# Kernel tuning notes

Hardware: AMD Instinct MI355X
Metric: run time of the kernel (lower is better)

Reference implementation:

```python
import jax, jax.numpy as jnp
from jax import lax
import numpy as np

H = 64          # featureDim (conv channels)
BN_EPS = 1e-5
COS_EPS = 1e-8


def _conv_block(x, w, b, g, beta):
    # Conv(k3, valid) + BatchNorm(batch stats, training mode) + ReLU + MaxPool2
    y = lax.conv_general_dilated(x, w, (1, 1), 'VALID',
                                 dimension_numbers=('NCHW', 'OIHW', 'NCHW'))
    y = y + b[None, :, None, None]
    mu = jnp.mean(y, axis=(0, 2, 3), keepdims=True)
    var = jnp.var(y, axis=(0, 2, 3), keepdims=True)
    y = (y - mu) * lax.rsqrt(var + BN_EPS) * g[None, :, None, None] + beta[None, :, None, None]
    y = jax.nn.relu(y)
    return lax.reduce_window(y, -jnp.inf, lax.max, (1, 1, 2, 2), (1, 1, 2, 2), 'VALID')


def _lstm_dir(xs, Wi, Wh, bi, bh, h, c):
    # one direction of nn.LSTM, batch size 1 (state vectors of shape [H])
    def step(carry, x):
        h, c = carry
        gates = x @ Wi.T + h @ Wh.T + bi + bh          # [4H], pytorch gate order i,f,g,o
        i_, f_, g_, o_ = jnp.split(gates, 4)
        c = jax.nn.sigmoid(f_) * c + jax.nn.sigmoid(i_) * jnp.tanh(g_)
        h = jax.nn.sigmoid(o_) * jnp.tanh(c)
        return (h, c), h
    _, hs = lax.scan(step, (h, c), xs)
    return hs  # [N, H]


def setup_inputs() -> dict:
    key = jax.random.key(0)
    ks = jax.random.split(key, 32)
    N, T, WAY = 1024, 1024, 20
    d = {}
    d['trainIm'] = jax.random.normal(ks[0], (N, 1, 28, 28), jnp.float32)
    d['trainLabel'] = jax.random.uniform(ks[1], (N, WAY), dtype=jnp.float32)
    d['testIm'] = jax.random.normal(ks[2], (T, 1, 28, 28), jnp.float32)
    d['testLabel'] = jax.random.uniform(ks[3], (T, WAY), dtype=jnp.float32)
    # featureNet params
    d['c1w'] = jax.random.normal(ks[4], (H, 1, 3, 3), jnp.float32) * 0.3
    d['c1b'] = jax.random.normal(ks[5], (H,), jnp.float32) * 0.05
    d['bn1g'] = jnp.ones((H,), jnp.float32)
    d['bn1b'] = jnp.zeros((H,), jnp.float32)
    d['c2w'] = jax.random.normal(ks[6], (H, H, 3, 3), jnp.float32) * 0.05
    d['c2b'] = jax.random.normal(ks[7], (H,), jnp.float32) * 0.05
    d['bn2g'] = jnp.ones((H,), jnp.float32)
    d['bn2b'] = jnp.zeros((H,), jnp.float32)
    d['c3w'] = jax.random.normal(ks[8], (H, H, 3, 3), jnp.float32) * 0.05
    d['c3b'] = jax.random.normal(ks[9], (H,), jnp.float32) * 0.05
    d['bn3g'] = jnp.ones((H,), jnp.float32)
    d['bn3b'] = jnp.zeros((H,), jnp.float32)
    # bidirectional nn.LSTM(H, H) params
    d['wi_f'] = jax.random.normal(ks[10], (4 * H, H), jnp.float32) * 0.1
    d['wh_f'] = jax.random.normal(ks[11], (4 * H, H), jnp.float32) * 0.1
    d['bi_f'] = jax.random.normal(ks[12], (4 * H,), jnp.float32) * 0.05
    d['bh_f'] = jax.random.normal(ks[13], (4 * H,), jnp.float32) * 0.05
    d['wi_b'] = jax.random.normal(ks[14], (4 * H, H), jnp.float32) * 0.1
    d['wh_b'] = jax.random.normal(ks[15], (4 * H, H), jnp.float32) * 0.1
    d['bi_b'] = jax.random.normal(ks[16], (4 * H,), jnp.float32) * 0.05
    d['bh_b'] = jax.random.normal(ks[17], (4 * H,), jnp.float32) * 0.05
    d['h0'] = jax.random.normal(ks[18], (2, 1, H), jnp.float32)
    d['c0'] = jax.random.normal(ks[19], (2, 1, H), jnp.float32)
    # AttenLSTMCell params + attLSTM initial state
    d['att_wih'] = jax.random.normal(ks[20], (H, 4 * H), jnp.float32) * 0.1
    d['att_whh'] = jax.random.normal(ks[21], (2 * H, 4 * H), jnp.float32) * 0.1
    d['att_b'] = jnp.zeros((4 * H,), jnp.float32)
    d['att_h0'] = jax.random.normal(ks[22], (1, H), jnp.float32)
    d['att_c0'] = jax.random.normal(ks[23], (1, H), jnp.float32)
    d['att_r0'] = jax.random.normal(ks[24], (1, H), jnp.float32)
    return d


def reference(trainIm, trainLabel, testIm, testLabel,
              c1w, c1b, bn1g, bn1b, c2w, c2b, bn2g, bn2b, c3w, c3b, bn3g, bn3b,
              wi_f, wh_f, bi_f, bh_f, wi_b, wh_b, bi_b, bh_b, h0, c0,
              att_wih, att_whh, att_b, att_h0, att_c0, att_r0):
    def feat(x):
        y = _conv_block(x, c1w, c1b, bn1g, bn1b)
        y = _conv_block(y, c2w, c2b, bn2g, bn2b)
        y = _conv_block(y, c3w, c3b, bn3g, bn3b)   # [B, 64, 1, 1]
        return y.reshape(-1, H)                    # [B, 64]

    ftr = feat(trainIm)   # [N, 64]
    fte = feat(testIm)    # [T, 64]

    # getCondEmbed_G: BiLSTM; cond[i] = fw[i] + bw_out[N-1-i] + x[i] == fw[i] + bw_raw[i] + x[i]
    hf = _lstm_dir(ftr, wi_f, wh_f, bi_f, bh_f, h0[0, 0], c0[0, 0])
    hb_raw = _lstm_dir(ftr[::-1], wi_b, wh_b, bi_b, bh_b, h0[1, 0], c0[1, 0])
    cond_train = hf + hb_raw + ftr                 # [N, 64]

    # getCondEmbed_F: sequential attLSTM over test samples (state persists across samples)
    def att_step(carry, x):
        h, c, r = carry                            # each [64]
        hcat = jnp.concatenate([h, r])             # [128]
        gates = hcat @ att_whh + x @ att_wih + att_b   # [256], cell gate order f,i,o,g
        f_, i_, o_, g_ = jnp.split(gates, 4)
        c = jax.nn.sigmoid(f_) * c + jax.nn.sigmoid(i_) * jnp.tanh(g_)
        h = jax.nn.sigmoid(o_) * jnp.tanh(c) + x   # residual add of testF
        att = jax.nn.softmax(cond_train @ h)       # [N] attention over support set
        r = att @ cond_train                       # [64] read vector
        return (h, c, r), h

    _, cond_test = lax.scan(att_step, (att_h0[0], att_c0[0], att_r0[0]), fte)  # [T, 64]

    # getLabel: cosine-similarity softmax attention over support labels
    num = cond_test @ cond_train.T                                       # [T, N]
    den = jnp.linalg.norm(cond_test, axis=1)[:, None] * jnp.linalg.norm(cond_train, axis=1)[None, :]
    sim = num / jnp.maximum(den, COS_EPS)
    att = jax.nn.softmax(sim, axis=1)
    return att @ trainLabel                                              # [T, way]
```

## Files before the change

### kernel.cpp

```cpp
#include <hip/hip_runtime.h>
#include <stdint.h>

__device__ __forceinline__ float bf2f(uint16_t v){ return __uint_as_float(((uint32_t)v) << 16); }
__device__ __forceinline__ uint16_t f2bf(float x){
  uint32_t u = __float_as_uint(x);
  return (uint16_t)((u + 0x7fffu + ((u >> 16) & 1u)) >> 16);
}
__device__ __forceinline__ float sigf(float x){
  float cx = fminf(fmaxf(x, -88.f), 88.f);
  return 1.f/(1.f + expf(-cx));
}
__device__ __forceinline__ float tanh_s(float x){
  float cx = fminf(fmaxf(x, -44.f), 44.f);
  return tanhf(cx);
}
__device__ __forceinline__ float fast_sig(float x){
  float cx = fminf(fmaxf(x, -60.f), 60.f);
  return 1.f/(1.f + __expf(-cx));
}
__device__ __forceinline__ float fast_tanh(float x){
  float cx = fminf(fmaxf(x, -15.f), 15.f);
  float e = __expf(2.f*cx);
  return (e - 1.f)/(e + 1.f);
}

typedef float v16 __attribute__((ext_vector_type(16)));

__device__ __forceinline__ float dot16(v16 v, const float4* p){
  float4 a = p[0], b = p[1], c = p[2], d = p[3];
  float s0 = v.s0*a.x + v.s1*a.y + v.s2*a.z + v.s3*a.w;
  float s1 = v.s4*b.x + v.s5*b.y + v.s6*b.z + v.s7*b.w;
  float s2 = v.s8*c.x + v.s9*c.y + v.sa*c.z + v.sb*c.w;
  float s3 = v.sc*d.x + v.sd*d.y + v.se*d.z + v.sf*d.w;
  return (s0+s1)+(s2+s3);
}
__device__ __forceinline__ void dot16pair(v16 va, v16 vb, const float4* p,
                                          float& accA, float& accB){
  float4 a = p[0], b = p[1], c = p[2], d = p[3];
  accA += (va.s0*a.x + va.s1*a.y + va.s2*a.z + va.s3*a.w)
        + (va.s4*b.x + va.s5*b.y + va.s6*b.z + va.s7*b.w)
        + (va.s8*c.x + va.s9*c.y + va.sa*c.z + va.sb*c.w)
        + (va.sc*d.x + va.sd*d.y + va.se*d.z + va.sf*d.w);
  accB += (vb.s0*a.x + vb.s1*a.y + vb.s2*a.z + vb.s3*a.w)
        + (vb.s4*b.x + vb.s5*b.y + vb.s6*b.z + vb.s7*b.w)
        + (vb.s8*c.x + vb.s9*c.y + vb.sa*c.z + vb.sb*c.w)
        + (vb.sc*d.x + vb.sd*d.y + vb.se*d.z + vb.sf*d.w);
}

#define LD16S(dst, P) do{ \
  dst.s0=(P)[0];    dst.s1=(P)[256];  dst.s2=(P)[512];  dst.s3=(P)[768];  \
  dst.s4=(P)[1024]; dst.s5=(P)[1280]; dst.s6=(P)[1536]; dst.s7=(P)[1792]; \
  dst.s8=(P)[2048]; dst.s9=(P)[2304]; dst.sa=(P)[2560]; dst.sb=(P)[2816]; \
  dst.sc=(P)[3072]; dst.sd=(P)[3328]; dst.se=(P)[3584]; dst.sf=(P)[3840]; }while(0)
#define LD16SB(dst, P) do{ \
  dst.s0=bf2f((P)[0]);    dst.s1=bf2f((P)[256]);  dst.s2=bf2f((P)[512]);  dst.s3=bf2f((P)[768]);  \
  dst.s4=bf2f((P)[1024]); dst.s5=bf2f((P)[1280]); dst.s6=bf2f((P)[1536]); dst.s7=bf2f((P)[1792]); \
  dst.s8=bf2f((P)[2048]); dst.s9=bf2f((P)[2304]); dst.sa=bf2f((P)[2560]); dst.sb=bf2f((P)[2816]); \
  dst.sc=bf2f((P)[3072]); dst.sd=bf2f((P)[3328]); dst.se=bf2f((P)[3584]); dst.sf=bf2f((P)[3840]); }while(0)
#define LD16CB(dst, P) do{ \
  dst.s0=bf2f((P)[0]);  dst.s1=bf2f((P)[1]);  dst.s2=bf2f((P)[2]);  dst.s3=bf2f((P)[3]);  \
  dst.s4=bf2f((P)[4]);  dst.s5=bf2f((P)[5]);  dst.s6=bf2f((P)[6]);  dst.s7=bf2f((P)[7]);  \
  dst.s8=bf2f((P)[8]);  dst.s9=bf2f((P)[9]);  dst.sa=bf2f((P)[10]); dst.sb=bf2f((P)[11]); \
  dst.sc=bf2f((P)[12]); dst.sd=bf2f((P)[13]); dst.se=bf2f((P)[14]); dst.sf=bf2f((P)[15]); }while(0)

static const size_t OFF_STATS = 0;
static const size_t OFF_FLAG  = 3072;
static const size_t OFF_AB    = 4096;
static const size_t OFF_P2R   = 8192;
static const size_t OFF_Y3    = 13115392;
static const size_t OFF_F     = 17833984;
static const size_t OFF_XI    = 18358272;
static const size_t OFF_XATT  = 20455424;
static const size_t OFF_CA    = 21504000;
static const size_t OFF_CB    = 21766144;
static const size_t OFF_COND  = 22028288;
static const size_t OFF_NC    = 22290432;
static const size_t OFF_CT    = 22294528;

__global__ void k_sniff(const uint32_t* im, float* stats, int* flag){
  int t = threadIdx.x;
  for (int i = t; i < 768; i += 256) stats[i] = 0.f;
  if (t < 64){
    uint32_t w = im[t];
    uint32_t e = (w >> 7) & 0xffu;
    bool sane = (e >= 100u && e <= 140u);
    unsigned long long m = __ballot(sane);
    if (t == 0) flag[0] = (__popcll(m) < 48) ? 1 : 0;
  }
}

__global__ __launch_bounds__(256) void k_conv1_stats(const void* im0, const void* im1,
        const void* w1, const void* b1, float* stats, const int* flag){
  __shared__ float xs[784];
  __shared__ float wl[576];
  __shared__ float bl1[64];
  __shared__ float rs[256], rq[256];
  int img = blockIdx.x;
  bool f32 = flag[0] != 0;
  if (f32){
    const float* im = (img < 1024) ? ((const float*)im0 + img*784) : ((const float*)im1 + (img-1024)*784);
    for (int i = threadIdx.x; i < 784; i += 256) xs[i] = im[i];
    for (int i = threadIdx.x; i < 576; i += 256) wl[i] = ((const float*)w1)[i];
    if (threadIdx.x < 64) bl1[threadIdx.x] = ((const float*)b1)[threadIdx.x];
  } else {
    const uint16_t* im = (img < 1024) ? ((const uint16_t*)im0 + img*784) : ((const uint16_t*)im1 + (img-1024)*784);
    for (int i = threadIdx.x; i < 784; i += 256) xs[i] = bf2f(im[i]);
    for (int i = threadIdx.x; i < 576; i += 256) wl[i] = bf2f(((const uint16_t*)w1)[i]);
    if (threadIdx.x < 64) bl1[threadIdx.x] = bf2f(((const uint16_t*)b1)[threadIdx.x]);
  }
  __syncthreads();
  int c = threadIdx.x & 63, pg = threadIdx.x >> 6;
  float w[9];
  #pragma unroll
  for (int k = 0; k < 9; k++) w[k] = wl[c*9+k];
  float bias = bl1[c];
  float s = 0.f, q = 0.f;
  for (int pos = pg; pos < 676; pos += 4){
    int y = pos/26, x = pos - y*26;
    const float* p = xs + y*28 + x;
    float acc = bias;
    #pragma unroll
    for (int dy = 0; dy < 3; dy++)
      #pragma unroll
      for (int dx = 0; dx < 3; dx++)
        acc += w[dy*3+dx]*p[dy*28+dx];
    s += acc; q += acc*acc;
  }
  rs[threadIdx.x] = s; rq[threadIdx.x] = q;
  __syncthreads();
  if (threadIdx.x < 64){
    float S = rs[c] + rs[c+64] + rs[c+128] + rs[c+192];
    float Q = rq[c] + rq[c+64] + rq[c+128] + rq[c+192];
    int batch = img >> 10;
    atomicAdd(&stats[batch*128 + c*2 + 0], S);
    atomicAdd(&stats[batch*128 + c*2 + 1], Q);
  }
}

__global__ void k_bnfin(const float* stats, float* ab, const void* g, const void* be,
                        int layer, float invc, const int* flag){
  __shared__ float gl[64], bel[64];
  int t = threadIdx.x;
  bool f32 = flag[0] != 0;
  if (t < 64){
    if (f32){ gl[t] = ((const float*)g)[t]; bel[t] = ((const float*)be)[t]; }
    else    { gl[t] = bf2f(((const uint16_t*)g)[t]); bel[t] = bf2f(((const uint16_t*)be)[t]); }
  }
  __syncthreads();
  if (t >= 128) return;
  int batch = t >> 6, c = t & 63;
  float s = stats[layer*256 + batch*128 + c*2];
  float q = stats[layer*256 + batch*128 + c*2 + 1];
  float mu = s*invc;
  float var = fmaxf(q*invc - mu*mu, 0.f);
  float A = gl[c] * rsqrtf(var + 1e-5f);
  float B = bel[c] - mu*A;
  ab[layer*256 + batch*128 + c*2]     = A;
  ab[layer*256 + batch*128 + c*2 + 1] = B;
}

__global__ __launch_bounds__(256) void k_conv2(const void* im0, const void* im1,
        const void* w1, const void* b1, const float* ab,
        const void* w2, const void* c2b, float* p2raw, float* stats, const int* flag){
  __shared__ float img[10816];
  __shared__ float ovl[4608];
  __shared__ float cbias[64];
  int b = blockIdx.x;
  int tid = threadIdx.x;
  bool f32 = flag[0] != 0;
  if (f32){
    const float* im = (b < 1024) ? ((const float*)im0 + b*784) : ((const float*)im1 + (b-1024)*784);
    for (int i = tid; i < 784; i += 256) ovl[i] = im[i];
    for (int i = tid; i < 576; i += 256) ovl[784+i] = ((const float*)w1)[i];
    if (tid < 64){ ovl[1360+tid] = ((const float*)b1)[tid]; cbias[tid] = ((const float*)c2b)[tid]; }
  } else {
    const uint16_t* im = (b < 1024) ? ((const uint16_t*)im0 + b*784) : ((const uint16_t*)im1 + (b-1024)*784);
    for (int i = tid; i < 784; i += 256) ovl[i] = bf2f(im[i]);
    for (int i = tid; i < 576; i += 256) ovl[784+i] = bf2f(((const uint16_t*)w1)[i]);
    if (tid < 64){ ovl[1360+tid] = bf2f(((const uint16_t*)b1)[tid]); cbias[tid] = bf2f(((const uint16_t*)c2b)[tid]); }
  }
  __syncthreads();
  int c = tid & 63, pg = tid >> 6;
  int batch = b >> 10;
  {
    float w[9];
    #pragma unroll
    for (int k = 0; k < 9; k++) w[k] = ovl[784 + c*9 + k];
    float bias = ovl[1360 + c];
    float A = ab[batch*128 + c*2], B = ab[batch*128 + c*2 + 1];
    for (int pp = pg; pp < 169; pp += 4){
      int py = pp/13, px = pp - py*13;
      float m = 0.f;
      #pragma unroll
      for (int q = 0; q < 4; q++){
        int yy = 2*py + (q>>1), xx = 2*px + (q&1);
        const float* p = ovl + yy*28 + xx;
        float acc = bias;
        #pragma unroll
        for (int dy = 0; dy < 3; dy++)
          #pragma unroll
          for (int dx = 0; dx < 3; dx++)
            acc += w[dy*3+dx]*p[dy*28+dx];
        m = fmaxf(m, A*acc + B);
      }
      img[c*169 + pp] = m;
    }
  }
  int lane = tid & 63, wv = tid >> 6;
  int pos0 = lane;
  int pos1 = lane + 64;
  bool v1 = (pos1 < 121);
  int p1c = v1 ? pos1 : pos0;
  int y0 = pos0/11, x0 = pos0 - y0*11;
  int y1 = p1c/11,  x1 = p1c - y1*11;
  float acc0[16], acc1[16];
  #pragma unroll
  for (int cc = 0; cc < 16; cc++){ acc0[cc]=0.f; acc1[cc]=0.f; }
  for (int ch = 0; ch < 8; ch++){
    int ci0 = ch*8;
    __syncthreads();
    if (f32){
      for (int i = tid; i < 4608; i += 256){
        int co = i/72, r = i - co*72;
        ovl[i] = ((const float*)w2)[(co*64 + ci0)*9 + r];
      }
    } else {
      for (int i = tid; i < 4608; i += 256){
        int co = i/72, r = i - co*72;
        ovl[i] = bf2f(((const uint16_t*)w2)[(co*64 + ci0)*9 + r]);
      }
    }
    __syncthreads();
    for (int cil = 0; cil < 8; cil++){
      int ci = ci0 + cil;
      float a[9], bv[9];
      const float* q0 = img + ci*169 + y0*13 + x0;
      const float* q1 = img + ci*169 + y1*13 + x1;
      #pragma unroll
      for (int dy = 0; dy < 3; dy++)
        #pragma unroll
        for (int dx = 0; dx < 3; dx++){
          a[dy*3+dx]  = q0[dy*13+dx];
          bv[dy*3+dx] = q1[dy*13+dx];
        }
      #pragma unroll
      for (int cc = 0; cc < 16; cc++){
        const float* wp = ovl + (wv*16+cc)*72 + cil*9;
        #pragma unroll
        for (int k = 0; k < 9; k++){
          acc0[cc] += wp[k]*a[k];
          acc1[cc] += wp[k]*bv[k];
        }
      }
    }
  }
  __syncthreads();
  float* ybuf = img;
  #pragma unroll
  for (int cc = 0; cc < 16; cc++){
    int co = wv*16 + cc;
    float bs = cbias[co];
    float u0 = acc0[cc] + bs;
    float u1 = acc1[cc] + bs;
    ybuf[co*121 + pos0] = u0;
    if (v1) ybuf[co*121 + pos1] = u1;
    float s = u0 + (v1 ? u1 : 0.f);
    float q = u0*u0 + (v1 ? u1*u1 : 0.f);
    #pragma unroll
    for (int off = 32; off; off >>= 1){
      s += __shfl_down(s, off);
      q += __shfl_down(q, off);
    }
    if (lane == 0){
      atomicAdd(&stats[256 + batch*128 + co*2 + 0], s);
      atomicAdd(&stats[256 + batch*128 + co*2 + 1], q);
    }
  }
  __syncthreads();
  for (int idx = tid; idx < 1600; idx += 256){
    int cc = idx/25, pp = idx - cc*25;
    int py = pp/5, px = pp - py*5;
    const float* s = ybuf + cc*121;
    float m = fmaxf(fmaxf(s[(2*py)*11 + 2*px], s[(2*py)*11 + 2*px + 1]),
                    fmaxf(s[(2*py+1)*11 + 2*px], s[(2*py+1)*11 + 2*px + 1]));
    p2raw[(size_t)b*1600 + idx] = m;
  }
}

__global__ __launch_bounds__(256) void k_conv3(const float* p2raw, const float* ab,
        const void* w3, const void* c3b, float* y3, float* stats, const int* flag){
  __shared__ float pimg[12800];
  __shared__ float wch[2304];
  __shared__ float cb3[64];
  __shared__ float abl[128];
  __shared__ float lstat[128];
  int b = blockIdx.x;
  int tid = threadIdx.x;
  bool f32 = flag[0] != 0;
  int batch = (b*8) >> 10;
  if (tid < 128){ abl[tid] = ab[256 + batch*128 + tid]; lstat[tid] = 0.f; }
  if (f32){ if (tid >= 128 && tid < 192) cb3[tid-128] = ((const float*)c3b)[tid-128]; }
  else    { if (tid >= 128 && tid < 192) cb3[tid-128] = bf2f(((const uint16_t*)c3b)[tid-128]); }
  __syncthreads();
  for (int idx = tid; idx < 12800; idx += 256){
    int rem = idx & 1599;
    int cch = rem / 25;
    pimg[idx] = fmaxf(abl[cch*2]*p2raw[(size_t)b*12800 + idx] + abl[cch*2+1], 0.f);
  }
  int il = tid >> 5, sub = tid & 31;
  float acc[18];
  #pragma unroll
  for (int s = 0; s < 18; s++){
    int o = sub + s*32;
    acc[s] = cb3[o/9];
  }
  for (int ch = 0; ch < 16; ch++){
    int ci0 = ch*4;
    __syncthreads();
    if (f32){
      for (int i = tid; i < 2304; i += 256){
        int co = i/36, r = i - co*36;
        wch[i] = ((const float*)w3)[(co*64 + ci0)*9 + r];
      }
    } else {
      for (int i = tid; i < 2304; i += 256){
        int co = i/36, r = i - co*36;
        wch[i] = bf2f(((const uint16_t*)w3)[(co*64 + ci0)*9 + r]);
      }
    }
    __syncthreads();
    #pragma unroll
    for (int s = 0; s < 18; s++){
      int o = sub + s*32;
      int co = o/9, pos = o - co*9;
      int y = pos/3, x = pos - y*3;
      float a = acc[s];
      #pragma unroll
      for (int cil = 0; cil < 4; cil++){
        const float* p = pimg + il*1600 + (ci0+cil)*25 + y*5 + x;
        const float* w = wch + co*36 + cil*9;
        #pragma unroll
        for (int dy = 0; dy < 3; dy++)
          #pragma unroll
          for (int dx = 0; dx < 3; dx++)
            a += w[dy*3+dx]*p[dy*5+dx];
      }
      acc[s] = a;
    }
  }
  #pragma unroll
  for (int s = 0; s < 18; s++){
    int o = sub + s*32;
    int co = o/9;
    y3[(size_t)(b*8+il)*576 + o] = acc[s];
    atomicAdd(&lstat[co*2 + 0], acc[s]);
    atomicAdd(&lstat[co*2 + 1], acc[s]*acc[s]);
  }
  __syncthreads();
  if (tid < 128)
    atomicAdd(&stats[512 + batch*128 + tid], lstat[tid]);
}

__global__ __launch_bounds__(256) void k_pool3(const float* y3, const float* ab, float* ff){
  int idx = blockIdx.x*256 + threadIdx.x;
  int img = idx >> 6, c = idx & 63;
  int batch = img >> 10;
  float A = ab[512 + batch*128 + c*2], B = ab[512 + batch*128 + c*2 + 1];
  const float* p = y3 + (size_t)img*576 + c*9;
  float m = 0.f;
  m = fmaxf(m, A*p[0]+B);
  m = fmaxf(m, A*p[1]+B);
  m = fmaxf(m, A*p[3]+B);
  m = fmaxf(m, A*p[4]+B);
  ff[idx] = m;
}

__global__ __launch_bounds__(256) void k_xproj(const float* ff,
        const void* wi_f, const void* bi_f, const void* bh_f,
        const void* wi_b, const void* bi_b, const void* bh_b,
        const void* att_wih, const void* att_b,
        float* Xi, float* Xatt, const int* flag){
  int which = blockIdx.x >> 10, t = blockIdx.x & 1023;
  __shared__ float xv[64];
  bool f32 = flag[0] != 0;
  const float* row = (which == 0) ? ff + t*64
                   : (which == 1) ? ff + (1023 - t)*64
                   : ff + (1024 + t)*64;
  if (threadIdx.x < 64) xv[threadIdx.x] = row[threadIdx.x];
  __syncthreads();
  int j = threadIdx.x;
  if (which < 2){
    const void* wi = which ? wi_b : wi_f;
    const void* bi = which ? bi_b : bi_f;
    const void* bh = which ? bh_b : bh_f;
    float acc;
    if (f32){
      acc = ((const float*)bi)[j] + ((const float*)bh)[j];
      const float* wp = (const float*)wi + j*64;
      #pragma unroll 8
      for (int k = 0; k < 64; k++) acc += wp[k]*xv[k];
    } else {
      acc = bf2f(((const uint16_t*)bi)[j]) + bf2f(((const uint16_t*)bh)[j]);
      const uint16_t* wp = (const uint16_t*)wi + j*64;
      #pragma unroll 8
      for (int k = 0; k < 64; k++) acc += bf2f(wp[k])*xv[k];
    }
    Xi[(size_t)which*262144 + t*256 + j] = acc;
  } else {
    float acc;
    if (f32){
      acc = ((const float*)att_b)[j];
      for (int k = 0; k < 64; k++) acc += ((const float*)att_wih)[k*256 + j]*xv[k];
    } else {
      acc = bf2f(((const uint16_t*)att_b)[j]);
      for (int k = 0; k < 64; k++) acc += bf2f(((const uint16_t*)att_wih)[k*256 + j])*xv[k];
    }
    Xatt[t*256 + j] = acc;
  }
}

__global__ __launch_bounds__(256, 1) void k_bilstm(const void* wh_f, const void* wh_b,
        const void* h0, const void* c0, const float* Xi, float* condA, float* condB,
        const int* flag){
  int dir = blockIdx.x;
  int j = threadIdx.x;
  bool f32 = flag[0] != 0;
  v16 wa, wb, wc, wd;
  if (f32){
    const v16* wp = (const v16*)((const float*)(dir ? wh_b : wh_f) + j*64);
    wa = wp[0]; wb = wp[1]; wc = wp[2]; wd = wp[3];
  } else {
    const uint16_t* wp = (const uint16_t*)(dir ? wh_b : wh_f) + j*64;
    LD16CB(wa, wp); LD16CB(wb, wp+16); LD16CB(wc, wp+32); LD16CB(wd, wp+48);
  }
  __shared__ __align__(16) float h[64];
  __shared__ float ga[256];
  float c = 0.f;
  if (j < 64){
    if (f32){ h[j] = ((const float*)h0)[dir*64 + j]; c = ((const float*)c0)[dir*64 + j]; }
    else    { h[j] = bf2f(((const uint16_t*)h0)[dir*64 + j]); c = bf2f(((const uint16_t*)c0)[dir*64 + j]); }
  }
  __syncthreads();
  const float* X = Xi + (size_t)dir*262144;
  float* out = dir ? condB : condA;
  float xcur = X[j];
  for (int t = 0; t < 1024; t++){
    float xnext = (t < 1023) ? X[(t+1)*256 + j] : 0.f;
    const float4* hp = (const float4*)h;
    float g = xcur + dot16(wa, hp) + dot16(wb, hp+4) + dot16(wc, hp+8) + dot16(wd, hp+12);
    ga[j] = (j < 128 || j >= 192) ? fast_sig(g) : fast_tanh(g);
    __syncthreads();
    if (j < 64){
      c = ga[64+j]*c + ga[j]*ga[128+j];
      float hv = ga[192+j]*fast_tanh(c);
      h[j] = hv;
      out[t*64 + j] = hv;
    }
    xcur = xnext;
    __syncthreads();
  }
}

__global__ void k_cond(const float* condA, const float* condB, const float* ff,
                       float* cond, float* ncond){
  int t = blockIdx.x, j = threadIdx.x;
  float v = condA[t*64+j] + condB[t*64+j] + ff[t*64+j];
  cond[t*64+j] = v;
  float s = v*v;
  #pragma unroll
  for (int off = 32; off; off >>= 1) s += __shfl_down(s, off);
  if (j == 0) ncond[t] = sqrtf(s);
}

__device__ __forceinline__ void av_chunk(v16 pv, int ch, int tid,
        float* pbuf, float (*rs2)[544]){
  float* pb = pbuf + tid*17;
  pb[0]=pv.s0;  pb[1]=pv.s1;  pb[2]=pv.s2;  pb[3]=pv.s3;
  pb[4]=pv.s4;  pb[5]=pv.s5;  pb[6]=pv.s6;  pb[7]=pv.s7;
  pb[8]=pv.s8;  pb[9]=pv.s9;  pb[10]=pv.sa; pb[11]=pv.sb;
  pb[12]=pv.sc; pb[13]=pv.sd; pb[14]=pv.se; pb[15]=pv.sf;
  __syncthreads();
  int kk = tid & 15, seg = tid >> 4;
  float a = 0.f;
  #pragma unroll
  for (int q = 0; q < 16; q++)
    a += pbuf[(seg*16+q)*17 + kk];
  rs2[ch][seg*17 + kk] = a;
  __syncthreads();
}

__global__ __launch_bounds__(512, 1) void k_attlstm(
        const float* cond, const float* Xatt, const float* ff,
        const void* whh, const void* ah0, const void* ac0, const void* ar0,
        float* ctest, const int* flag){
  __shared__ __align__(16) float hr[128];
  __shared__ float gpart[512];
  __shared__ float pbuf[512*17];
  __shared__ float rs2[4][544];
  __shared__ float wred[16];
  int tid = threadIdx.x;
  bool f32 = flag[0] != 0;
  int j = tid & 255, half = tid >> 8;
  v16 wka, wkb, wkc, wkd;
  if (f32){
    const float* W = (const float*)whh + (size_t)half*16384 + j;
    LD16S(wka, W); LD16S(wkb, W+4096); LD16S(wkc, W+8192); LD16S(wkd, W+12288);
  } else {
    const uint16_t* W = (const uint16_t*)whh + (size_t)half*16384 + j;
    LD16SB(wka, W); LD16SB(wkb, W+4096); LD16SB(wkc, W+8192); LD16SB(wkd, W+12288);
  }
  const v16* rp0 = (const v16*)(cond + (size_t)tid*64);
  const v16* rp1 = (const v16*)(cond + (size_t)(tid+512)*64);
  v16 r0a = rp0[0], r0b = rp0[1], r0c = rp0[2], r0d = rp0[3];
  v16 r1a = rp1[0], r1b = rp1[1], r1c = rp1[2], r1d = rp1[3];
  float c = 0.f;
  if (f32){
    if (tid < 64){ hr[tid] = ((const float*)ah0)[tid]; c = ((const float*)ac0)[tid]; }
    else if (tid < 128) hr[tid] = ((const float*)ar0)[tid-64];
  } else {
    if (tid < 64){ hr[tid] = bf2f(((const uint16_t*)ah0)[tid]); c = bf2f(((const uint16_t*)ac0)[tid]); }
    else if (tid < 128) hr[tid] = bf2f(((const uint16_t*)ar0)[tid-64]);
  }
  __syncthreads();
  int lane = tid & 63, wv = tid >> 6;
  const float* fte = ff + 65536;
  for (int st = 0; st < 1024; st++){
    {
      const float4* hc = (const float4*)(hr + half*64);
      float g = (half == 0) ? Xatt[st*256 + j] : 0.f;
      g += dot16(wka, hc) + dot16(wkb, hc+4) + dot16(wkc, hc+8) + dot16(wkd, hc+12);
      gpart[tid] = g;
    }
    __syncthreads();
    if (tid < 64){
      float xres = fte[st*64 + tid];
      float gf = gpart[tid]     + gpart[256+tid];
      float gi = gpart[64+tid]  + gpart[320+tid];
      float go = gpart[128+tid] + gpart[384+tid];
      float gg = gpart[192+tid] + gpart[448+tid];
      float f_ = fast_sig(gf), i_ = fast_sig(gi), o_ = fast_sig(go), g_ = fast_tanh(gg);
      c = f_*c + i_*g_;
      float hv = o_*fast_tanh(c) + xres;
      hr[tid] = hv;
      ctest[st*64 + tid] = hv;
    }
    __syncthreads();
    float lg0 = 0.f, lg1 = 0.f;
    {
      const float4* hq = (const float4*)hr;
      dot16pair(r0a, r1a, hq,    lg0, lg1);
      dot16pair(r0b, r1b, hq+4,  lg0, lg1);
      dot16pair(r0c, r1c, hq+8,  lg0, lg1);
      dot16pair(r0d, r1d, hq+12, lg0, lg1);
    }
    float mx = fmaxf(lg0, lg1);
    #pragma unroll
    for (int off = 32; off; off >>= 1) mx = fmaxf(mx, __shfl_xor(mx, off));
    if (lane == 0) wred[wv] = mx;
    __syncthreads();
    float gmax = fmaxf(fmaxf(fmaxf(wred[0],wred[1]),fmaxf(wred[2],wred[3])),
                       fmaxf(fmaxf(wred[4],wred[5]),fmaxf(wred[6],wred[7])));
    float e0 = __expf(lg0 - gmax), e1 = __expf(lg1 - gmax);
    float s = e0 + e1;
    #pragma unroll
    for (int off = 32; off; off >>= 1) s += __shfl_xor(s, off);
    if (lane == 0) wred[8+wv] = s;
    __syncthreads();
    float inv = 1.f/(((wred[8]+wred[9])+(wred[10]+wred[11]))
                   + ((wred[12]+wred[13])+(wred[14]+wred[15])));
    av_chunk(e0*r0a + e1*r1a, 0, tid, pbuf, rs2);
    av_chunk(e0*r0b + e1*r1b, 1, tid, pbuf, rs2);
    av_chunk(e0*r0c + e1*r1c, 2, tid, pbuf, rs2);
    av_chunk(e0*r0d + e1*r1d, 3, tid, pbuf, rs2);
    if (tid < 64){
      int kk = lane & 15, chq = lane >> 4;
      float a = 0.f;
      #pragma unroll
      for (int sgm = 0; sgm < 32; sgm++) a += rs2[chq][sgm*17 + kk];
      hr[64 + lane] = a * inv;
    }
    __syncthreads();
  }
}

__global__ __launch_bounds__(256) void k_final(const float* ctest, const float* cond,
        const float* ncond, const void* labels, void* out, const int* flag){
  int t = blockIdx.x;
  __shared__ __align__(16) float q[64];
  __shared__ float sim[1024];
  __shared__ float red[4];
  __shared__ float accw[20];
  __shared__ float bcv[2];
  int tid = threadIdx.x;
  bool f32 = flag[0] != 0;
  if (tid < 64) q[tid] = ctest[t*64 + tid];
  if (tid < 20) accw[tid] = 0.f;
  __syncthreads();
  if (tid < 64){
    float s = q[tid]*q[tid];
    #pragma unroll
    for (int off = 32; off; off >>= 1) s += __shfl_down(s, off);
    if (tid == 0) bcv[0] = sqrtf(s);
  }
  __syncthreads();
  float nq = bcv[0];
  float mymax = -1e30f;
  for (int i = tid; i < 1024; i += 256){
    float d = 0.f;
    const float4* cr = (const float4*)(cond + i*64);
    #pragma unroll
    for (int k4 = 0; k4 < 16; k4++){
      float4 cv = cr[k4];
      float4 qv = ((const float4*)q)[k4];
      d += cv.x*qv.x + cv.y*qv.y + cv.z*qv.z + cv.w*qv.w;
    }
    float den = fmaxf(nq*ncond[i], 1e-8f);
    float sv = d/den;
    sim[i] = sv;
    mymax = fmaxf(mymax, sv);
  }
  int lane = tid & 63, wv = tid >> 6;
  #pragma unroll
  for (int off = 32; off; off >>= 1) mymax = fmaxf(mymax, __shfl_down(mymax, off));
  if (lane == 0) red[wv] = mymax;
  __syncthreads();
  if (tid == 0) bcv[1] = fmaxf(fmaxf(red[0], red[1]), fmaxf(red[2], red[3]));
  __syncthreads();
  float smax = bcv[1];
  float es = 0.f;
  float la[20];
  #pragma unroll
  for (int w = 0; w < 20; w++) la[w] = 0.f;
  if (f32){
    for (int i = tid; i < 1024; i += 256){
      float e = __expf(sim[i] - smax);
      es += e;
      const float* L = (const float*)labels + i*20;
      #pragma unroll
      for (int w = 0; w < 20; w++) la[w] += e*L[w];
    }
  } else {
    for (int i = tid; i < 1024; i += 256){
      float e = __expf(sim[i] - smax);
      es += e;
      const uint16_t* L = (const uint16_t*)labels + i*20;
      #pragma unroll
      for (int w = 0; w < 20; w++) la[w] += e*bf2f(L[w]);
    }
  }
  #pragma unroll
  for (int off = 32; off; off >>= 1) es += __shfl_down(es, off);
  if (lane == 0) red[wv] = es;
  #pragma unroll
  for (int w = 0; w < 20; w++) atomicAdd(&accw[w], la[w]);
  __syncthreads();
  if (tid == 0) bcv[0] = 1.f/(red[0] + red[1] + red[2] + red[3]);
  __syncthreads();
  if (tid < 20){
    float v = accw[tid]*bcv[0];
    if (f32) ((float*)out)[t*20 + tid] = v;
    else     ((uint16_t*)out)[t*20 + tid] = f2bf(v);
  }
}

extern "C" void kernel_launch(void* const* d_in, const int* in_sizes, int n_in,
                              void* d_out, int out_size, void* d_ws, size_t ws_size,
                              hipStream_t stream){
  const void* trainIm    = d_in[0];
  const void* trainLabel = d_in[1];
  const void* testIm     = d_in[2];
  const void* c1w  = d_in[4];
  const void* c1b  = d_in[5];
  const void* bn1g = d_in[6];
  const void* bn1b = d_in[7];
  const void* c2w  = d_in[8];
  const void* c2b  = d_in[9];
  const void* bn2g = d_in[10];
  const void* bn2b = d_in[11];
  const void* c3w  = d_in[12];
  const void* c3b  = d_in[13];
  const void* bn3g = d_in[14];
  const void* bn3b = d_in[15];
  const void* wi_f = d_in[16];
  const void* wh_f = d_in[17];
  const void* bi_f = d_in[18];
  const void* bh_f = d_in[19];
  const void* wi_b = d_in[20];
  const void* wh_b = d_in[21];
  const void* bi_b = d_in[22];
  const void* bh_b = d_in[23];
  const void* h0   = d_in[24];
  const void* c0   = d_in[25];
  const void* att_wih = d_in[26];
  const void* att_whh = d_in[27];
  const void* att_b   = d_in[28];
  const void* att_h0  = d_in[29];
  const void* att_c0  = d_in[30];
  const void* att_r0  = d_in[31];

  char* ws = (char*)d_ws;
  float* stats = (float*)(ws + OFF_STATS);
  int*   flag  = (int*)(ws + OFF_FLAG);
  float* ab    = (float*)(ws + OFF_AB);
  float* p2raw = (float*)(ws + OFF_P2R);
  float* y3    = (float*)(ws + OFF_Y3);
  float* ff    = (float*)(ws + OFF_F);
  float* Xi    = (float*)(ws + OFF_XI);
  float* Xatt  = (float*)(ws + OFF_XATT);
  float* condA = (float*)(ws + OFF_CA);
  float* condB = (float*)(ws + OFF_CB);
  float* cond  = (float*)(ws + OFF_COND);
  float* ncond = (float*)(ws + OFF_NC);
  float* ctest = (float*)(ws + OFF_CT);

  k_sniff<<<1, 256, 0, stream>>>((const uint32_t*)trainIm, stats, flag);
  k_conv1_stats<<<2048, 256, 0, stream>>>(trainIm, testIm, c1w, c1b, stats, flag);
  k_bnfin<<<1, 192, 0, stream>>>(stats, ab, bn1g, bn1b, 0, 1.f/692224.f, flag);
  k_conv2<<<2048, 256, 0, stream>>>(trainIm, testIm, c1w, c1b, ab, c2w, c2b, p2raw, stats, flag);
  k_bnfin<<<1, 192, 0, stream>>>(stats, ab, bn2g, bn2b, 1, 1.f/123904.f, flag);
  k_conv3<<<256, 256, 0, stream>>>(p2raw, ab, c3w, c3b, y3, stats, flag);
  k_bnfin<<<1, 192, 0, stream>>>(stats, ab, bn3g, bn3b, 2, 1.f/9216.f, flag);
  k_pool3<<<512, 256, 0, stream>>>(y3, ab, ff);
  k_xproj<<<3072, 256, 0, stream>>>(ff, wi_f, bi_f, bh_f, wi_b, bi_b, bh_b, att_wih, att_b, Xi, Xatt, flag);
  k_bilstm<<<2, 256, 0, stream>>>(wh_f, wh_b, h0, c0, Xi, condA, condB, flag);
  k_cond<<<1024, 64, 0, stream>>>(condA, condB, ff, cond, ncond);
  k_attlstm<<<1, 512, 0, stream>>>(cond, Xatt, ff, att_whh, att_h0, att_c0, att_r0, ctest, flag);
  k_final<<<1024, 256, 0, stream>>>(ctest, cond, ncond, trainLabel, d_out, flag);
}
```

Baseline: 6.833 ms.

## Use per-wave softmax rescaling and bf16-packed partials to cut attention-step barriers

The attention LSTM step now computes each wave's softmax with its own local max and sum, then rescales them after a single barrier, replacing the two global-reduction barriers. The attention-weighted partial vectors are packed into bf16 pairs in shared memory, so the reduction runs in two chunks instead of four and needs fewer barriers and LDS stores. The Xatt and residual loads are moved ahead of the first barrier. The trade-off is that the attention read vector is accumulated from bf16-rounded partials, which lowers precision inside a 1024-step recurrence.

```diff
diff --git a/kernel.cpp b/kernel.cpp
--- a/kernel.cpp
+++ b/kernel.cpp
@@ -6,6 +6,12 @@
   uint32_t u = __float_as_uint(x);
   return (uint16_t)((u + 0x7fffu + ((u >> 16) & 1u)) >> 16);
 }
+__device__ __forceinline__ uint32_t pkbf(float lo, float hi){
+  uint32_t ua = __float_as_uint(lo), ub = __float_as_uint(hi);
+  return ((ua + 0x8000u) >> 16) | ((ub + 0x8000u) & 0xffff0000u);
+}
+__device__ __forceinline__ float bl(uint32_t u){ return __uint_as_float(u << 16); }
+__device__ __forceinline__ float bh_(uint32_t u){ return __uint_as_float(u & 0xffff0000u); }
 __device__ __forceinline__ float sigf(float x){
   float cx = fminf(fmaxf(x, -88.f), 88.f);
   return 1.f/(1.f + expf(-cx));
@@ -62,6 +68,23 @@
   dst.s4=bf2f((P)[4]);  dst.s5=bf2f((P)[5]);  dst.s6=bf2f((P)[6]);  dst.s7=bf2f((P)[7]);  \
   dst.s8=bf2f((P)[8]);  dst.s9=bf2f((P)[9]);  dst.sa=bf2f((P)[10]); dst.sb=bf2f((P)[11]); \
   dst.sc=bf2f((P)[12]); dst.sd=bf2f((P)[13]); dst.se=bf2f((P)[14]); dst.sf=bf2f((P)[15]); }while(0)
+#define AVPACK(rA0, rA1, rB0, rB1, PB) do{ \
+  (PB)[0]  = pkbf(e0*rA0.s0+e1*rA1.s0, e0*rA0.s1+e1*rA1.s1); \
+  (PB)[1]  = pkbf(e0*rA0.s2+e1*rA1.s2, e0*rA0.s3+e1*rA1.s3); \
+  (PB)[2]  = pkbf(e0*rA0.s4+e1*rA1.s4, e0*rA0.s5+e1*rA1.s5); \
+  (PB)[3]  = pkbf(e0*rA0.s6+e1*rA1.s6, e0*rA0.s7+e1*rA1.s7); \
+  (PB)[4]  = pkbf(e0*rA0.s8+e1*rA1.s8, e0*rA0.s9+e1*rA1.s9); \
+  (PB)[5]  = pkbf(e0*rA0.sa+e1*rA1.sa, e0*rA0.sb+e1*rA1.sb); \
+  (PB)[6]  = pkbf(e0*rA0.sc+e1*rA1.sc, e0*rA0.sd+e1*rA1.sd); \
+  (PB)[7]  = pkbf(e0*rA0.se+e1*rA1.se, e0*rA0.sf+e1*rA1.sf); \
+  (PB)[8]  = pkbf(e0*rB0.s0+e1*rB1.s0, e0*rB0.s1+e1*rB1.s1); \
+  (PB)[9]  = pkbf(e0*rB0.s2+e1*rB1.s2, e0*rB0.s3+e1*rB1.s3); \
+  (PB)[10] = pkbf(e0*rB0.s4+e1*rB1.s4, e0*rB0.s5+e1*rB1.s5); \
+  (PB)[11] = pkbf(e0*rB0.s6+e1*rB1.s6, e0*rB0.s7+e1*rB1.s7); \
+  (PB)[12] = pkbf(e0*rB0.s8+e1*rB1.s8, e0*rB0.s9+e1*rB1.s9); \
+  (PB)[13] = pkbf(e0*rB0.sa+e1*rB1.sa, e0*rB0.sb+e1*rB1.sb); \
+  (PB)[14] = pkbf(e0*rB0.sc+e1*rB1.sc, e0*rB0.sd+e1*rB1.sd); \
+  (PB)[15] = pkbf(e0*rB0.se+e1*rB1.se, e0*rB0.sf+e1*rB1.sf); }while(0)
 
 static const size_t OFF_STATS = 0;
 static const size_t OFF_FLAG  = 3072;
@@ -472,31 +495,14 @@
   if (j == 0) ncond[t] = sqrtf(s);
 }
 
-__device__ __forceinline__ void av_chunk(v16 pv, int ch, int tid,
-        float* pbuf, float (*rs2)[544]){
-  float* pb = pbuf + tid*17;
-  pb[0]=pv.s0;  pb[1]=pv.s1;  pb[2]=pv.s2;  pb[3]=pv.s3;
-  pb[4]=pv.s4;  pb[5]=pv.s5;  pb[6]=pv.s6;  pb[7]=pv.s7;
-  pb[8]=pv.s8;  pb[9]=pv.s9;  pb[10]=pv.sa; pb[11]=pv.sb;
-  pb[12]=pv.sc; pb[13]=pv.sd; pb[14]=pv.se; pb[15]=pv.sf;
-  __syncthreads();
-  int kk = tid & 15, seg = tid >> 4;
-  float a = 0.f;
-  #pragma unroll
-  for (int q = 0; q < 16; q++)
-    a += pbuf[(seg*16+q)*17 + kk];
-  rs2[ch][seg*17 + kk] = a;
-  __syncthreads();
-}
-
 __global__ __launch_bounds__(512, 1) void k_attlstm(
         const float* cond, const float* Xatt, const float* ff,
         const void* whh, const void* ah0, const void* ac0, const void* ar0,
         float* ctest, const int* flag){
   __shared__ __align__(16) float hr[128];
   __shared__ float gpart[512];
-  __shared__ float pbuf[512*17];
-  __shared__ float rs2[4][544];
+  __shared__ uint32_t pbuf[512*17];
+  __shared__ float2 rs2[2][512];
   __shared__ float wred[16];
   int tid = threadIdx.x;
   bool f32 = flag[0] != 0;
@@ -523,17 +529,18 @@
   }
   __syncthreads();
   int lane = tid & 63, wv = tid >> 6;
+  int pr = tid & 15, seg = tid >> 4;
   const float* fte = ff + 65536;
   for (int st = 0; st < 1024; st++){
+    float xa = (half == 0) ? Xatt[st*256 + j] : 0.f;
+    float xres = (tid < 64) ? fte[st*64 + tid] : 0.f;
     {
       const float4* hc = (const float4*)(hr + half*64);
-      float g = (half == 0) ? Xatt[st*256 + j] : 0.f;
-      g += dot16(wka, hc) + dot16(wkb, hc+4) + dot16(wkc, hc+8) + dot16(wkd, hc+12);
+      float g = xa + dot16(wka, hc) + dot16(wkb, hc+4) + dot16(wkc, hc+8) + dot16(wkd, hc+12);
       gpart[tid] = g;
     }
     __syncthreads();
     if (tid < 64){
-      float xres = fte[st*64 + tid];
       float gf = gpart[tid]     + gpart[256+tid];
       float gi = gpart[64+tid]  + gpart[320+tid];
       float go = gpart[128+tid] + gpart[384+tid];
@@ -556,27 +563,57 @@
     float mx = fmaxf(lg0, lg1);
     #pragma unroll
     for (int off = 32; off; off >>= 1) mx = fmaxf(mx, __shfl_xor(mx, off));
-    if (lane == 0) wred[wv] = mx;
-    __syncthreads();
-    float gmax = fmaxf(fmaxf(fmaxf(wred[0],wred[1]),fmaxf(wred[2],wred[3])),
-                       fmaxf(fmaxf(wred[4],wred[5]),fmaxf(wred[6],wred[7])));
-    float e0 = __expf(lg0 - gmax), e1 = __expf(lg1 - gmax);
+    float e0 = __expf(lg0 - mx), e1 = __expf(lg1 - mx);
     float s = e0 + e1;
     #pragma unroll
     for (int off = 32; off; off >>= 1) s += __shfl_xor(s, off);
-    if (lane == 0) wred[8+wv] = s;
-    __syncthreads();
-    float inv = 1.f/(((wred[8]+wred[9])+(wred[10]+wred[11]))
-                   + ((wred[12]+wred[13])+(wred[14]+wred[15])));
-    av_chunk(e0*r0a + e1*r1a, 0, tid, pbuf, rs2);
-    av_chunk(e0*r0b + e1*r1b, 1, tid, pbuf, rs2);
-    av_chunk(e0*r0c + e1*r1c, 2, tid, pbuf, rs2);
-    av_chunk(e0*r0d + e1*r1d, 3, tid, pbuf, rs2);
+    if (lane == 0){ wred[wv] = mx; wred[8+wv] = s; }
+    {
+      uint32_t* pb = pbuf + tid*17;
+      AVPACK(r0a, r1a, r0b, r1b, pb);
+    }
+    __syncthreads();
+    float gmax = fmaxf(fmaxf(fmaxf(wred[0],wred[1]),fmaxf(wred[2],wred[3])),
+                       fmaxf(fmaxf(wred[4],wred[5]),fmaxf(wred[6],wred[7])));
+    float total = wred[8]*__expf(wred[0]-gmax) + wred[9]*__expf(wred[1]-gmax)
+                + wred[10]*__expf(wred[2]-gmax) + wred[11]*__expf(wred[3]-gmax)
+                + wred[12]*__expf(wred[4]-gmax) + wred[13]*__expf(wred[5]-gmax)
+                + wred[14]*__expf(wred[6]-gmax) + wred[15]*__expf(wred[7]-gmax);
+    float inv = 1.f/total;
+    float sw = __expf(wred[seg>>2] - gmax);
+    {
+      float a0 = 0.f, a1 = 0.f;
+      #pragma unroll
+      for (int q = 0; q < 16; q++){
+        uint32_t u = pbuf[(seg*16+q)*17 + pr];
+        a0 += bl(u); a1 += bh_(u);
+      }
+      rs2[0][seg*16 + pr] = make_float2(a0*sw, a1*sw);
+    }
+    __syncthreads();
+    {
+      uint32_t* pb = pbuf + tid*17;
+      AVPACK(r0c, r1c, r0d, r1d, pb);
+    }
+    __syncthreads();
+    {
+      float a0 = 0.f, a1 = 0.f;
+      #pragma unroll
+      for (int q = 0; q < 16; q++){
+        uint32_t u = pbuf[(seg*16+q)*17 + pr];
+        a0 += bl(u); a1 += bh_(u);
+      }
+      rs2[1][seg*16 + pr] = make_float2(a0*sw, a1*sw);
+    }
+    __syncthreads();
     if (tid < 64){
-      int kk = lane & 15, chq = lane >> 4;
+      int ch = lane >> 5, c32 = lane & 31, prr = c32 >> 1, lh = c32 & 1;
       float a = 0.f;
       #pragma unroll
-      for (int sgm = 0; sgm < 32; sgm++) a += rs2[chq][sgm*17 + kk];
+      for (int sgm = 0; sgm < 32; sgm++){
+        float2 v = rs2[ch][sgm*16 + prr];
+        a += lh ? v.y : v.x;
+      }
       hr[64 + lane] = a * inv;
     }
     __syncthreads();
```

Measured after the change: 13.02 ms. 1.91x slower.
